# Kernel optimization log

Hardware: AMD Instinct MI355X
Metric: run time of the kernel (lower is better)

Reference implementation:

```python
import jax, jax.numpy as jnp
import numpy as np

# config constants (match init_kwargs)
D_MODEL = 1024        # hidden_size
D_FF = 2048           # intermediate_size
N_EXPERTS = 8         # num_local_experts
TOP_K = 2             # num_experts_per_tok


def setup_inputs() -> dict:
    key = jax.random.key(0)
    k1, k2, k3, k4 = jax.random.split(key, 4)
    layer_input = jax.random.normal(k1, (2, 2048, D_MODEL), dtype=jnp.float32)
    # router: nn.Linear(hidden_size, num_experts, bias=False) -> weight [E, D]
    router_weight = jax.random.normal(k2, (N_EXPERTS, D_MODEL), dtype=jnp.float32) * 0.02
    # ParallelExperts weights: [num_experts, out_features, in_features]
    w_in = jax.random.normal(k3, (N_EXPERTS, 2 * D_FF, D_MODEL), dtype=jnp.float32) * 0.02
    w_out = jax.random.normal(k4, (N_EXPERTS, D_MODEL, D_FF), dtype=jnp.float32) * 0.02
    return {"layer_input": layer_input, "router_weight": router_weight,
            "w_in": w_in, "w_out": w_out}


def _moe_forward(x, router_weight, w_in, w_out):
    # x: [T, D]
    T = x.shape[0]
    logits = x @ router_weight.T                       # [T, E] router logits
    top_vals, top_idx = jax.lax.top_k(logits, TOP_K)   # [T, K]
    gates_k = jax.nn.softmax(top_vals, axis=-1).astype(x.dtype)
    # dense gate matrix: zero for unselected experts -> identical math to
    # the gather / grouped-GEMM / scatter-add path in the torch module.
    gates = jnp.zeros((T, N_EXPERTS), x.dtype).at[
        jnp.arange(T)[:, None], top_idx].set(gates_k)  # [T, E]
    # grouped GEMM #1: [E, T, 2*D_FF]
    h = jnp.einsum('td,efd->etf', x, w_in)
    h1, h2 = jnp.split(h, 2, axis=-1)
    act = jax.nn.silu(h1) * h2                         # SwiGLU: silu(a)*b
    # grouped GEMM #2: [E, T, D]
    y = jnp.einsum('eth,edh->etd', act, w_out)
    # gate-weighted combine (scatter-add equivalent)
    out = jnp.einsum('etd,te->td', y, gates)           # [T, D]
    return out, logits


def reference(layer_input, router_weight, w_in, w_out):
    bsz, length, emb = layer_input.shape
    x = layer_input.reshape(-1, emb)
    out, router_logits = _moe_forward(x, router_weight, w_in, w_out)
    return out.reshape(bsz, length, emb), router_logits
```

## Files before the change

### kernel.cpp

```cpp
#include <hip/hip_runtime.h>
#include <stdint.h>

#define N_TOK   4096
#define DMODEL  1024
#define DFF     2048
#define N_EXP   8
#define N_SLOTS (N_TOK * 2)
#define ROWS_PAD (N_SLOTS + 128)
#define MAX_TILES 72

typedef __bf16 bf16x8 __attribute__((ext_vector_type(8)));
typedef float  f32x4  __attribute__((ext_vector_type(4)));
typedef unsigned short u16;
typedef unsigned short u16x4 __attribute__((ext_vector_type(4)));

__device__ __forceinline__ u16 f2bf(float f) {
    union { float f; uint32_t u; } v; v.f = f;
    uint32_t r = v.u + 0x7FFFu + ((v.u >> 16) & 1u);
    return (u16)(r >> 16);
}
__device__ __forceinline__ float bf2f(u16 u) {
    union { uint32_t u; float f; } v; v.u = ((uint32_t)u) << 16;
    return v.f;
}

__device__ __forceinline__ u16x4 f2bf4(float4 a) {
    union { uint32_t w[2]; u16x4 o; } u;
    asm("v_cvt_pk_bf16_f32 %0, %1, %2" : "=v"(u.w[0]) : "v"(a.x), "v"(a.y));
    asm("v_cvt_pk_bf16_f32 %0, %1, %2" : "=v"(u.w[1]) : "v"(a.z), "v"(a.w));
    return u.o;
}

__device__ __forceinline__ void g2l16(const void* gp, void* lp) {
    auto g = reinterpret_cast<const __attribute__((address_space(1))) unsigned int*>(
        reinterpret_cast<uintptr_t>(gp));
    auto l = reinterpret_cast<__attribute__((address_space(3))) unsigned int*>(
        reinterpret_cast<uintptr_t>(lp));
    __builtin_amdgcn_global_load_lds(g, l, 16, 0, 0);
}

__device__ __forceinline__ int idx64(int r, int cb) {
    return r * 64 + ((cb ^ (r & 7)) * 8);
}

#define RTR_BLOCKS (N_TOK / 4)

__global__ void router_kernel(const float* __restrict__ x, const float* __restrict__ rw,
                              float* __restrict__ logits, int* __restrict__ tok_expert,
                              float* __restrict__ tok_gate) {
    int t = blockIdx.x * 4 + (threadIdx.x >> 6);
    int lane = threadIdx.x & 63;
    const float* xr = x + (size_t)t * DMODEL;
    float acc[N_EXP];
#pragma unroll
    for (int e = 0; e < N_EXP; ++e) acc[e] = 0.f;
    for (int i = 0; i < DMODEL / 64; ++i) {
        int k = lane + i * 64;
        float xv = xr[k];
#pragma unroll
        for (int e = 0; e < N_EXP; ++e) acc[e] += xv * rw[e * DMODEL + k];
    }
#pragma unroll
    for (int e = 0; e < N_EXP; ++e) {
        float v = acc[e];
        for (int off = 32; off > 0; off >>= 1) v += __shfl_down(v, off, 64);
        acc[e] = v;
    }
    if (lane == 0) {
        float* lg = logits + (size_t)t * N_EXP;
#pragma unroll
        for (int e = 0; e < N_EXP; ++e) lg[e] = acc[e];
        int e0 = 0; float v0 = acc[0];
#pragma unroll
        for (int e = 1; e < N_EXP; ++e) if (acc[e] > v0) { v0 = acc[e]; e0 = e; }
        int e1 = -1; float v1 = -3.0e38f;
#pragma unroll
        for (int e = 0; e < N_EXP; ++e) if (e != e0 && acc[e] > v1) { v1 = acc[e]; e1 = e; }
        float ex = expf(v1 - v0);
        tok_expert[t * 2 + 0] = e0;  tok_gate[t * 2 + 0] = 1.0f / (1.0f + ex);
        tok_expert[t * 2 + 1] = e1;  tok_gate[t * 2 + 1] = ex / (1.0f + ex);
    }
}

__global__ void scan_kernel(const int* __restrict__ tok_expert, int* __restrict__ offs,
                            int* __restrict__ inv, int* __restrict__ tiletab) {
    __shared__ int cnt[N_EXP][257];
    __shared__ int soffs[N_EXP];
    int tid = threadIdx.x;
    int base = tid * 32;
    int loc[N_EXP];
#pragma unroll
    for (int e = 0; e < N_EXP; ++e) loc[e] = 0;
    for (int i = 0; i < 32; ++i) {
        int ex = tok_expert[base + i];
#pragma unroll
        for (int e = 0; e < N_EXP; ++e) loc[e] += (ex == e);
    }
#pragma unroll
    for (int e = 0; e < N_EXP; ++e) cnt[e][tid] = loc[e];
    __syncthreads();
    if (tid < N_EXP) {
        int running = 0;
        for (int t = 0; t < 256; ++t) { int c = cnt[tid][t]; cnt[tid][t] = running; running += c; }
        cnt[tid][256] = running;
    }
    __syncthreads();
    if (tid == 0) {
        int s = 0;
        for (int e = 0; e < N_EXP; ++e) { offs[e] = s; soffs[e] = s; s += cnt[e][256]; }
        offs[N_EXP] = s;
        int n = 0;
        for (int e = 0; e < N_EXP; ++e) {
            int c = cnt[e][256];
            int r0 = soffs[e];
            for (int m = 0; m * 128 < c; ++m) {
                int rem = c - m * 128;
                tiletab[4 + n * 4 + 0] = e;
                tiletab[4 + n * 4 + 1] = r0 + m * 128;
                tiletab[4 + n * 4 + 2] = rem < 128 ? rem : 128;
                ++n;
            }
        }
        tiletab[0] = n;
    }
    __syncthreads();
#pragma unroll
    for (int e = 0; e < N_EXP; ++e) loc[e] = 0;
    for (int i = 0; i < 32; ++i) {
        int ex = tok_expert[base + i];
        int row = 0;
#pragma unroll
        for (int e = 0; e < N_EXP; ++e)
            if (ex == e) { row = soffs[e] + cnt[e][tid] + loc[e]; loc[e]++; }
        inv[base + i] = row;
    }
}

__global__ void gather_kernel(const float* __restrict__ x, const int* __restrict__ inv,
                              u16* __restrict__ Abf) {
    int t = blockIdx.x;
    int r0 = inv[t * 2];
    int r1 = inv[t * 2 + 1];
    float4 v = ((const float4*)(x + (size_t)t * DMODEL))[threadIdx.x];
    u16x4 o = { f2bf(v.x), f2bf(v.y), f2bf(v.z), f2bf(v.w) };
    *(u16x4*)(Abf + (size_t)r0 * DMODEL + threadIdx.x * 4) = o;
    *(u16x4*)(Abf + (size_t)r1 * DMODEL + threadIdx.x * 4) = o;
}

__global__ __launch_bounds__(256, 3)
void gemm1_kernel(const u16* __restrict__ Abf, const float* __restrict__ win,
                  u16* __restrict__ act, const int* __restrict__ tiletab) {
    int bid = blockIdx.x;
    int nt = bid & 31;
    int ti = bid >> 5;
    if (ti >= tiletab[0]) return;
    int e    = tiletab[4 + ti * 4 + 0];
    int row0 = tiletab[4 + ti * 4 + 1];
    int mmax = tiletab[4 + ti * 4 + 2];
    int n0 = nt * 64;
    const float* wsrc = win + (size_t)e * (2 * DFF) * DMODEL;

    __shared__ u16 lsA[128 * 64];
    __shared__ u16 lsB[2][64 * 64];

    int tid = threadIdx.x, lane = tid & 63, wave = tid >> 6;
    int wm = wave >> 1, wn = wave & 1;
    int s_r8 = lane >> 3;
    int s_cb = ((lane & 7) ^ (lane >> 3)) * 8;
    int lr4 = lane >> 4;
    int lc  = lane & 15;
    int cbs = lc >> 1;
    int hf  = (lane & 1) * 4;

    f32x4 acc[2][4][2];
    f32x4 zero = {0.f, 0.f, 0.f, 0.f};
#pragma unroll
    for (int h = 0; h < 2; ++h)
#pragma unroll
        for (int mi = 0; mi < 4; ++mi)
#pragma unroll
            for (int ni = 0; ni < 2; ++ni) acc[h][mi][ni] = zero;

    for (int kk = 0; kk < DMODEL / 64; ++kk) {
        int k0 = kk * 64;
        float4 v[2][4];
#pragma unroll
        for (int h = 0; h < 2; ++h)
#pragma unroll
            for (int q2 = 0; q2 < 4; ++q2)
                v[h][q2] = *(const float4*)(wsrc +
                    (size_t)(h * DFF + n0 + wave * 16 + q2 * 4 + lr4) * DMODEL + k0 + lc * 4);
#pragma unroll
        for (int q = 0; q < 4; ++q) {
            int R0 = wave * 32 + q * 8;
            g2l16(Abf + (size_t)(row0 + R0 + s_r8) * DMODEL + k0 + s_cb, &lsA[R0 * 64]);
        }
#pragma unroll
        for (int h = 0; h < 2; ++h)
#pragma unroll
            for (int q2 = 0; q2 < 4; ++q2) {
                int r = wave * 16 + q2 * 4 + lr4;
                *(u16x4*)&lsB[h][idx64(r, cbs) + hf] = f2bf4(v[h][q2]);
            }
        __syncthreads();
#pragma unroll
        for (int kh = 0; kh < 2; ++kh) {
            int cb = kh * 4 + (lane >> 4);
            bf16x8 afr[4];
#pragma unroll
            for (int mi = 0; mi < 4; ++mi)
                afr[mi] = *(const bf16x8*)&lsA[idx64(wm * 64 + mi * 16 + (lane & 15), cb)];
#pragma unroll
            for (int h = 0; h < 2; ++h)
#pragma unroll
                for (int ni = 0; ni < 2; ++ni) {
                    bf16x8 bfr = *(const bf16x8*)&lsB[h][idx64(wn * 32 + ni * 16 + (lane & 15), cb)];
#pragma unroll
                    for (int mi = 0; mi < 4; ++mi)
                        acc[h][mi][ni] = __builtin_amdgcn_mfma_f32_16x16x32_bf16(
                            afr[mi], bfr, acc[h][mi][ni], 0, 0, 0);
                }
        }
        __syncthreads();
    }
#pragma unroll
    for (int mi = 0; mi < 4; ++mi)
#pragma unroll
        for (int i = 0; i < 4; ++i) {
            int rl = wm * 64 + mi * 16 + (lane >> 4) * 4 + i;
            if (rl < mmax) {
                size_t rp = (size_t)(row0 + rl) * DFF;
#pragma unroll
                for (int ni = 0; ni < 2; ++ni) {
                    int col = n0 + wn * 32 + ni * 16 + (lane & 15);
                    float a = acc[0][mi][ni][i];
                    float b = acc[1][mi][ni][i];
                    float sv = a / (1.0f + __expf(-a));
                    act[rp + col] = f2bf(sv * b);
                }
            }
        }
}

__global__ __launch_bounds__(256, 3)
void gemm2_kernel(const u16* __restrict__ act, const float* __restrict__ wout,
                  u16* __restrict__ ybA, u16* __restrict__ ybB,
                  const int* __restrict__ tiletab) {
    int bid = blockIdx.x;
    int kc = bid & 1;
    int nt = (bid >> 1) & 7;
    int ti = bid >> 4;
    if (ti >= tiletab[0]) return;
    int e    = tiletab[4 + ti * 4 + 0];
    int row0 = tiletab[4 + ti * 4 + 1];
    int mmax = tiletab[4 + ti * 4 + 2];
    int n0 = nt * 128;
    const float* wsrc = wout + (size_t)e * DMODEL * DFF;

    __shared__ u16 lsA[128 * 64];
    __shared__ u16 lsB[128 * 64];

    int tid = threadIdx.x, lane = tid & 63, wave = tid >> 6;
    int wm = wave >> 1, wn = wave & 1;
    int s_r8 = lane >> 3;
    int s_cb = ((lane & 7) ^ (lane >> 3)) * 8;
    int lr4 = lane >> 4;
    int lc  = lane & 15;
    int cbs = lc >> 1;
    int hf  = (lane & 1) * 4;
    u16* yb = kc ? ybB : ybA;

    f32x4 acc[4][4];
    f32x4 zero = {0.f, 0.f, 0.f, 0.f};
#pragma unroll
    for (int mi = 0; mi < 4; ++mi)
#pragma unroll
        for (int ni = 0; ni < 4; ++ni) acc[mi][ni] = zero;

    for (int kk = kc * 16; kk < kc * 16 + 16; ++kk) {
        int k0 = kk * 64;
#pragma unroll
        for (int g = 0; g < 2; ++g) {
            float4 v[4];
#pragma unroll
            for (int q2 = 0; q2 < 4; ++q2)
                v[q2] = *(const float4*)(wsrc +
                    (size_t)(n0 + wave * 32 + g * 16 + q2 * 4 + lr4) * DFF + k0 + lc * 4);
            if (g == 0) {
#pragma unroll
                for (int q = 0; q < 4; ++q) {
                    int R0 = wave * 32 + q * 8;
                    g2l16(act + (size_t)(row0 + R0 + s_r8) * DFF + k0 + s_cb, &lsA[R0 * 64]);
                }
            }
#pragma unroll
            for (int q2 = 0; q2 < 4; ++q2) {
                int r = wave * 32 + g * 16 + q2 * 4 + lr4;
                *(u16x4*)&lsB[idx64(r, cbs) + hf] = f2bf4(v[q2]);
            }
        }
        __syncthreads();
#pragma unroll
        for (int kh = 0; kh < 2; ++kh) {
            int cb = kh * 4 + (lane >> 4);
            bf16x8 afr[4];
#pragma unroll
            for (int mi = 0; mi < 4; ++mi)
                afr[mi] = *(const bf16x8*)&lsA[idx64(wm * 64 + mi * 16 + (lane & 15), cb)];
#pragma unroll
            for (int ni = 0; ni < 4; ++ni) {
                bf16x8 bfr = *(const bf16x8*)&lsB[idx64(wn * 64 + ni * 16 + (lane & 15), cb)];
#pragma unroll
                for (int mi = 0; mi < 4; ++mi)
                    acc[mi][ni] = __builtin_amdgcn_mfma_f32_16x16x32_bf16(
                        afr[mi], bfr, acc[mi][ni], 0, 0, 0);
            }
        }
        __syncthreads();
    }
#pragma unroll
    for (int mi = 0; mi < 4; ++mi)
#pragma unroll
        for (int i = 0; i < 4; ++i) {
            int rl = wm * 64 + mi * 16 + (lane >> 4) * 4 + i;
            if (rl < mmax) {
                u16* yrow = yb + (size_t)(row0 + rl) * DMODEL;
#pragma unroll
                for (int ni = 0; ni < 4; ++ni) {
                    int col = n0 + wn * 64 + ni * 16 + (lane & 15);
                    yrow[col] = f2bf(acc[mi][ni][i]);
                }
            }
        }
}

__global__ void combine_kernel(const u16* __restrict__ ybA, const u16* __restrict__ ybB,
                               const int* __restrict__ inv, const float* __restrict__ tok_gate,
                               float* __restrict__ out) {
    int t = blockIdx.x;
    int tid = threadIdx.x;
    __shared__ int sr0, sr1;
    __shared__ float sg0, sg1;
    if (tid == 0) {
        sr0 = inv[t * 2];  sr1 = inv[t * 2 + 1];
        sg0 = tok_gate[t * 2];  sg1 = tok_gate[t * 2 + 1];
    }
    __syncthreads();
    int d = tid * 4;
    u16x4 a0 = *(const u16x4*)(ybA + (size_t)sr0 * DMODEL + d);
    u16x4 b0 = *(const u16x4*)(ybB + (size_t)sr0 * DMODEL + d);
    u16x4 a1 = *(const u16x4*)(ybA + (size_t)sr1 * DMODEL + d);
    u16x4 b1 = *(const u16x4*)(ybB + (size_t)sr1 * DMODEL + d);
    float4 o;
    o.x = sg0 * (bf2f(a0.x) + bf2f(b0.x)) + sg1 * (bf2f(a1.x) + bf2f(b1.x));
    o.y = sg0 * (bf2f(a0.y) + bf2f(b0.y)) + sg1 * (bf2f(a1.y) + bf2f(b1.y));
    o.z = sg0 * (bf2f(a0.z) + bf2f(b0.z)) + sg1 * (bf2f(a1.z) + bf2f(b1.z));
    o.w = sg0 * (bf2f(a0.w) + bf2f(b0.w)) + sg1 * (bf2f(a1.w) + bf2f(b1.w));
    *(float4*)(out + (size_t)t * DMODEL + d) = o;
}

extern "C" void kernel_launch(void* const* d_in, const int* in_sizes, int n_in,
                              void* d_out, int out_size, void* d_ws, size_t ws_size,
                              hipStream_t stream) {
    const float* x    = (const float*)d_in[0];
    const float* rw   = (const float*)d_in[1];
    const float* win  = (const float*)d_in[2];
    const float* wout = (const float*)d_in[3];
    float* out    = (float*)d_out;
    float* logits = out + (size_t)N_TOK * DMODEL;

    char* ws = (char*)d_ws;
    size_t o = 0;
    auto alloc = [&](size_t bytes) -> void* {
        void* p = ws + o;
        o = (o + bytes + 255) & ~(size_t)255;
        return p;
    };
    u16*   Abf      = (u16*)  alloc((size_t)ROWS_PAD * DMODEL * 2);
    u16*   actbuf   = (u16*)  alloc((size_t)ROWS_PAD * DFF * 2);
    u16*   ybA      = (u16*)  alloc((size_t)ROWS_PAD * DMODEL * 2);
    u16*   ybB      = (u16*)  alloc((size_t)ROWS_PAD * DMODEL * 2);
    int*   offs     = (int*)  alloc(16 * 4);
    int*   inv      = (int*)  alloc(N_SLOTS * 4);
    int*   tok_exp  = (int*)  alloc(N_SLOTS * 4);
    float* tok_gate = (float*)alloc(N_SLOTS * 4);
    int*   tiletab  = (int*)  alloc((4 + MAX_TILES * 4) * 4);
    (void)ws_size; (void)in_sizes; (void)n_in; (void)out_size;

    router_kernel<<<RTR_BLOCKS, 256, 0, stream>>>(x, rw, logits, tok_exp, tok_gate);
    scan_kernel<<<1, 256, 0, stream>>>(tok_exp, offs, inv, tiletab);
    gather_kernel<<<N_TOK, 256, 0, stream>>>(x, inv, Abf);
    gemm1_kernel<<<MAX_TILES * 32, 256, 0, stream>>>(Abf, win, actbuf, tiletab);
    gemm2_kernel<<<MAX_TILES * 16, 256, 0, stream>>>(actbuf, wout, ybA, ybB, tiletab);
    combine_kernel<<<N_TOK, 256, 0, stream>>>(ybA, ybB, inv, tok_gate, out);
}
```

Baseline: 502.9 us.

## Load fp32 weights directly to LDS asynchronously and convert to bf16 at fragment read

Both GEMM kernels now stream the fp32 expert weight tiles straight into shared memory with global_load_lds, using an XOR swizzle, instead of loading them into registers, converting to bf16 and storing to LDS. The bf16 conversion moves to the point where each MFMA B fragment is read from LDS. This removes the register staging and VGPR pressure of the weight path and lets the weight loads run asynchronously. In exchange the weight tile takes twice the LDS, which may lower occupancy, and each B fragment is converted again for every wave that reads it.

After: 434.3 us. -13.7%, faster.

```diff
diff --git a/kernel.cpp b/kernel.cpp
--- a/kernel.cpp
+++ b/kernel.cpp
@@ -24,10 +24,12 @@
     return v.f;
 }
 
-__device__ __forceinline__ u16x4 f2bf4(float4 a) {
-    union { uint32_t w[2]; u16x4 o; } u;
-    asm("v_cvt_pk_bf16_f32 %0, %1, %2" : "=v"(u.w[0]) : "v"(a.x), "v"(a.y));
-    asm("v_cvt_pk_bf16_f32 %0, %1, %2" : "=v"(u.w[1]) : "v"(a.z), "v"(a.w));
+__device__ __forceinline__ bf16x8 cvt8(f32x4 lo, f32x4 hi) {
+    union { uint32_t w[4]; bf16x8 o; } u;
+    asm("v_cvt_pk_bf16_f32 %0, %1, %2" : "=v"(u.w[0]) : "v"(lo[0]), "v"(lo[1]));
+    asm("v_cvt_pk_bf16_f32 %0, %1, %2" : "=v"(u.w[1]) : "v"(lo[2]), "v"(lo[3]));
+    asm("v_cvt_pk_bf16_f32 %0, %1, %2" : "=v"(u.w[2]) : "v"(hi[0]), "v"(hi[1]));
+    asm("v_cvt_pk_bf16_f32 %0, %1, %2" : "=v"(u.w[3]) : "v"(hi[2]), "v"(hi[3]));
     return u.o;
 }
 
@@ -160,17 +162,15 @@
     int n0 = nt * 64;
     const float* wsrc = win + (size_t)e * (2 * DFF) * DMODEL;
 
-    __shared__ u16 lsA[128 * 64];
-    __shared__ u16 lsB[2][64 * 64];
+    __shared__ u16   lsA[128 * 64];
+    __shared__ float lsBf[2][64 * 64];
 
     int tid = threadIdx.x, lane = tid & 63, wave = tid >> 6;
     int wm = wave >> 1, wn = wave & 1;
     int s_r8 = lane >> 3;
     int s_cb = ((lane & 7) ^ (lane >> 3)) * 8;
-    int lr4 = lane >> 4;
-    int lc  = lane & 15;
-    int cbs = lc >> 1;
-    int hf  = (lane & 1) * 4;
+    int f_r4 = lane >> 4;
+    int l15  = lane & 15;
 
     f32x4 acc[2][4][2];
     f32x4 zero = {0.f, 0.f, 0.f, 0.f};
@@ -183,13 +183,6 @@
 
     for (int kk = 0; kk < DMODEL / 64; ++kk) {
         int k0 = kk * 64;
-        float4 v[2][4];
-#pragma unroll
-        for (int h = 0; h < 2; ++h)
-#pragma unroll
-            for (int q2 = 0; q2 < 4; ++q2)
-                v[h][q2] = *(const float4*)(wsrc +
-                    (size_t)(h * DFF + n0 + wave * 16 + q2 * 4 + lr4) * DMODEL + k0 + lc * 4);
 #pragma unroll
         for (int q = 0; q < 4; ++q) {
             int R0 = wave * 32 + q * 8;
@@ -198,23 +191,32 @@
 #pragma unroll
         for (int h = 0; h < 2; ++h)
 #pragma unroll
-            for (int q2 = 0; q2 < 4; ++q2) {
-                int r = wave * 16 + q2 * 4 + lr4;
-                *(u16x4*)&lsB[h][idx64(r, cbs) + hf] = f2bf4(v[h][q2]);
+            for (int q = 0; q < 4; ++q) {
+                int R0 = wave * 16 + q * 4;
+                int rl = R0 + f_r4;
+                int sb = l15 ^ (rl & 15);
+                g2l16(wsrc + (size_t)(h * DFF + n0 + rl) * DMODEL + k0 + sb * 4,
+                      &lsBf[h][R0 * 64]);
             }
         __syncthreads();
 #pragma unroll
         for (int kh = 0; kh < 2; ++kh) {
-            int cb = kh * 4 + (lane >> 4);
+            int g  = lane >> 4;
+            int cb = kh * 4 + g;
             bf16x8 afr[4];
 #pragma unroll
             for (int mi = 0; mi < 4; ++mi)
-                afr[mi] = *(const bf16x8*)&lsA[idx64(wm * 64 + mi * 16 + (lane & 15), cb)];
+                afr[mi] = *(const bf16x8*)&lsA[idx64(wm * 64 + mi * 16 + l15, cb)];
 #pragma unroll
             for (int h = 0; h < 2; ++h)
 #pragma unroll
                 for (int ni = 0; ni < 2; ++ni) {
-                    bf16x8 bfr = *(const bf16x8*)&lsB[h][idx64(wn * 32 + ni * 16 + (lane & 15), cb)];
+                    int r  = wn * 32 + ni * 16 + l15;
+                    int rx = r & 15;
+                    int sb0 = cb * 2;
+                    f32x4 lo = *(const f32x4*)&lsBf[h][r * 64 + ((sb0     ^ rx) * 4)];
+                    f32x4 hi = *(const f32x4*)&lsBf[h][r * 64 + (((sb0+1) ^ rx) * 4)];
+                    bf16x8 bfr = cvt8(lo, hi);
 #pragma unroll
                     for (int mi = 0; mi < 4; ++mi)
                         acc[h][mi][ni] = __builtin_amdgcn_mfma_f32_16x16x32_bf16(
@@ -232,7 +234,7 @@
                 size_t rp = (size_t)(row0 + rl) * DFF;
 #pragma unroll
                 for (int ni = 0; ni < 2; ++ni) {
-                    int col = n0 + wn * 32 + ni * 16 + (lane & 15);
+                    int col = n0 + wn * 32 + ni * 16 + l15;
                     float a = acc[0][mi][ni][i];
                     float b = acc[1][mi][ni][i];
                     float sv = a / (1.0f + __expf(-a));
@@ -257,17 +259,15 @@
     int n0 = nt * 128;
     const float* wsrc = wout + (size_t)e * DMODEL * DFF;
 
-    __shared__ u16 lsA[128 * 64];
-    __shared__ u16 lsB[128 * 64];
+    __shared__ u16   lsA[128 * 64];
+    __shared__ float lsBf[128 * 64];
 
     int tid = threadIdx.x, lane = tid & 63, wave = tid >> 6;
     int wm = wave >> 1, wn = wave & 1;
     int s_r8 = lane >> 3;
     int s_cb = ((lane & 7) ^ (lane >> 3)) * 8;
-    int lr4 = lane >> 4;
-    int lc  = lane & 15;
-    int cbs = lc >> 1;
-    int hf  = (lane & 1) * 4;
+    int f_r4 = lane >> 4;
+    int l15  = lane & 15;
     u16* yb = kc ? ybB : ybA;
 
     f32x4 acc[4][4];
@@ -280,36 +280,34 @@
     for (int kk = kc * 16; kk < kc * 16 + 16; ++kk) {
         int k0 = kk * 64;
 #pragma unroll
-        for (int g = 0; g < 2; ++g) {
-            float4 v[4];
-#pragma unroll
-            for (int q2 = 0; q2 < 4; ++q2)
-                v[q2] = *(const float4*)(wsrc +
-                    (size_t)(n0 + wave * 32 + g * 16 + q2 * 4 + lr4) * DFF + k0 + lc * 4);
-            if (g == 0) {
-#pragma unroll
-                for (int q = 0; q < 4; ++q) {
-                    int R0 = wave * 32 + q * 8;
-                    g2l16(act + (size_t)(row0 + R0 + s_r8) * DFF + k0 + s_cb, &lsA[R0 * 64]);
-                }
-            }
-#pragma unroll
-            for (int q2 = 0; q2 < 4; ++q2) {
-                int r = wave * 32 + g * 16 + q2 * 4 + lr4;
-                *(u16x4*)&lsB[idx64(r, cbs) + hf] = f2bf4(v[q2]);
-            }
+        for (int q = 0; q < 4; ++q) {
+            int R0 = wave * 32 + q * 8;
+            g2l16(act + (size_t)(row0 + R0 + s_r8) * DFF + k0 + s_cb, &lsA[R0 * 64]);
+        }
+#pragma unroll
+        for (int q = 0; q < 8; ++q) {
+            int R0 = wave * 32 + q * 4;
+            int rl = R0 + f_r4;
+            int sb = l15 ^ (rl & 15);
+            g2l16(wsrc + (size_t)(n0 + rl) * DFF + k0 + sb * 4, &lsBf[R0 * 64]);
         }
         __syncthreads();
 #pragma unroll
         for (int kh = 0; kh < 2; ++kh) {
-            int cb = kh * 4 + (lane >> 4);
+            int g  = lane >> 4;
+            int cb = kh * 4 + g;
             bf16x8 afr[4];
 #pragma unroll
             for (int mi = 0; mi < 4; ++mi)
-                afr[mi] = *(const bf16x8*)&lsA[idx64(wm * 64 + mi * 16 + (lane & 15), cb)];
+                afr[mi] = *(const bf16x8*)&lsA[idx64(wm * 64 + mi * 16 + l15, cb)];
 #pragma unroll
             for (int ni = 0; ni < 4; ++ni) {
-                bf16x8 bfr = *(const bf16x8*)&lsB[idx64(wn * 64 + ni * 16 + (lane & 15), cb)];
+                int r  = wn * 64 + ni * 16 + l15;
+                int rx = r & 15;
+                int sb0 = cb * 2;
+                f32x4 lo = *(const f32x4*)&lsBf[r * 64 + ((sb0     ^ rx) * 4)];
+                f32x4 hi = *(const f32x4*)&lsBf[r * 64 + (((sb0+1) ^ rx) * 4)];
+                bf16x8 bfr = cvt8(lo, hi);
 #pragma unroll
                 for (int mi = 0; mi < 4; ++mi)
                     acc[mi][ni] = __builtin_amdgcn_mfma_f32_16x16x32_bf16(
@@ -327,7 +325,7 @@
                 u16* yrow = yb + (size_t)(row0 + rl) * DMODEL;
 #pragma unroll
                 for (int ni = 0; ni < 4; ++ni) {
-                    int col = n0 + wn * 64 + ni * 16 + (lane & 15);
+                    int col = n0 + wn * 64 + ni * 16 + l15;
                     yrow[col] = f2bf(acc[mi][ni][i]);
                 }
             }
```
